# Optimization experiments

Hardware: AMD Instinct MI355X
Metric: run time of the kernel (lower is better)

The kernel has to match this reference:

```python
import jax, jax.numpy as jnp
import numpy as np

WINDOW_SIZE = 7
CHANNEL = 1
SIGMA = 1.5


def _create_window(window_size=WINDOW_SIZE, channel=CHANNEL):
    coords = jnp.arange(window_size, dtype=jnp.float32) - window_size // 2
    g = jnp.exp(-coords ** 2 / (2.0 * SIGMA ** 2))
    g = g / g.sum()
    w2d = g[:, None] * g[None, :]                      # [K, K]
    # depthwise kernel, OIHW with I=1 (groups=channel)
    return jnp.broadcast_to(w2d[None, None], (channel, 1, window_size, window_size))


def _dwconv(x, window):
    pad = WINDOW_SIZE // 2
    return jax.lax.conv_general_dilated(
        x, window,
        window_strides=(1, 1),
        padding=[(pad, pad), (pad, pad)],
        dimension_numbers=('NCHW', 'OIHW', 'NCHW'),
        feature_group_count=CHANNEL,
    )


def setup_inputs() -> dict:
    key = jax.random.key(0)
    k1, k2 = jax.random.split(key)
    shape = (128, CHANNEL, 256, 256)
    pred = jax.random.uniform(k1, shape, dtype=jnp.float32)
    target = jax.random.uniform(k2, shape, dtype=jnp.float32)
    window = _create_window()
    return {"pred": pred, "target": target, "window": window}


def reference(pred, target, window):
    C1 = 0.01 ** 2
    C2 = 0.03 ** 2
    mu1 = _dwconv(pred, window)
    mu2 = _dwconv(target, window)
    mu1_sq = mu1 * mu1
    mu2_sq = mu2 * mu2
    mu12 = mu1 * mu2
    sigma1_sq = _dwconv(pred * pred, window) - mu1_sq
    sigma2_sq = _dwconv(target * target, window) - mu2_sq
    sigma12 = _dwconv(pred * target, window) - mu12
    ssim_map = ((2.0 * mu12 + C1) * (2.0 * sigma12 + C2)) / (
        (mu1_sq + mu2_sq + C1) * (sigma1_sq + sigma2_sq + C2))
    return 1.0 - ssim_map.mean()
```

## Files before the change

kernel.cpp:

```cpp
#include <hip/hip_runtime.h>

#define IMG_H 256
#define IMG_W 256
#define ROWS 16
#define NIMG 128
#define NWAVES (NIMG * (IMG_H / ROWS) * 2)

__device__ __forceinline__ float ssim1(float mu1, float mu2, float spp, float stt, float spt) {
    const float C1 = 1e-4f, C2 = 9e-4f;
    float mu1s = mu1 * mu1, mu2s = mu2 * mu2, mu12 = mu1 * mu2;
    float s1 = spp - mu1s, s2 = stt - mu2s, s12 = spt - mu12;
    float num = (2.f * mu12 + C1) * (2.f * s12 + C2);
    float den = (mu1s + mu2s + C1) * (s1 + s2 + C2);
    return num * __builtin_amdgcn_rcpf(den);
}

template<int ATOMIC>
__global__ __launch_bounds__(256) void ssim_main(
    const float* __restrict__ pred,
    const float* __restrict__ targ,
    const float* __restrict__ window,
    float* __restrict__ wsum)
{
    __shared__ float2 sbuf[4][136];

    const int lane = threadIdx.x & 63;
    const int wid  = threadIdx.x >> 6;
    const int gw   = blockIdx.x * 4 + wid;
    const int n    = gw >> 5;
    const int r    = gw & 31;
    const int r0   = (r >> 1) * ROWS;
    const int X0   = (r & 1) << 7;

    float g[7];
    {
        float sum = 0.f;
#pragma unroll
        for (int j = 0; j < 7; ++j) { g[j] = window[21 + j]; sum += g[j]; }
        float inv = 1.f / sum;
#pragma unroll
        for (int j = 0; j < 7; ++j) g[j] *= inv;
    }

    const float* pimg = pred + (size_t)n * (IMG_H * IMG_W);
    const float* timg = targ + (size_t)n * (IMG_H * IMG_W);
    const int mo = X0 + 2 * lane;

    int hidx = 0, hcol = 0;
    if (lane < 3)      { hidx = lane + 1;   hcol = X0 - 3 + lane;   }
    else if (lane < 6) { hidx = lane + 129; hcol = X0 + 125 + lane; }
    const bool hv = (lane < 6) && ((unsigned)hcol < (unsigned)IMG_W);

    float Amu[7], Atu[7], App[7], Att[7], Apt[7];
    float Bmu[7], Btu[7], Bpp[7], Btt[7], Bpt[7];
    float acc = 0.f;

    float2 Pr, Tr, Hr;

#define GLOAD(J) { \
    const int j_ = (J); \
    Pr = make_float2(0.f, 0.f); Tr = Pr; Hr = Pr; \
    if ((unsigned)j_ < (unsigned)IMG_H) { \
        Pr = *(const float2*)(pimg + j_ * IMG_W + mo); \
        Tr = *(const float2*)(timg + j_ * IMG_W + mo); \
        if (hv) { \
            Hr.x = pimg[j_ * IMG_W + hcol]; \
            Hr.y = timg[j_ * IMG_W + hcol]; \
        } \
    } }

#define TAP(K, P, T) { \
    float wp = g[K] * (P), wt = g[K] * (T); \
    m_  = fmaf(g[K], (P), m_);  u_  = fmaf(g[K], (T), u_); \
    pp_ = fmaf(wp, (P), pp_);   tt_ = fmaf(wt, (T), tt_); \
    pt_ = fmaf(wp, (T), pt_); }

#define HC(SLOT, MU, TU, PP, TT, PT, p0,p1,p2,p3,p4,p5,p6, t0,t1,t2,t3,t4,t5,t6) { \
    float m_ = 0.f, u_ = 0.f, pp_ = 0.f, tt_ = 0.f, pt_ = 0.f; \
    TAP(0, p0, t0) TAP(1, p1, t1) TAP(2, p2, t2) TAP(3, p3, t3) \
    TAP(4, p4, t4) TAP(5, p5, t5) TAP(6, p6, t6) \
    MU[SLOT] = m_; TU[SLOT] = u_; PP[SLOT] = pp_; TT[SLOT] = tt_; PT[SLOT] = pt_; }

#define VD(A_, U) ( fmaf(g[6], A_[((U)+6)%7], fmaf(g[5], A_[((U)+5)%7], \
    fmaf(g[4], A_[((U)+4)%7], fmaf(g[3], A_[((U)+3)%7], fmaf(g[2], A_[((U)+2)%7], \
    fmaf(g[1], A_[((U)+1)%7], g[0] * A_[(U)%7])))))) )

#define OUTR(U) { \
    { float m1 = VD(Amu,U), m2 = VD(Atu,U), pp = VD(App,U), tt = VD(Att,U), pt = VD(Apt,U); \
      acc += ssim1(m1, m2, pp, tt, pt); } \
    { float m1 = VD(Bmu,U), m2 = VD(Btu,U), pp = VD(Bpp,U), tt = VD(Btt,U), pt = VD(Bpt,U); \
      acc += ssim1(m1, m2, pp, tt, pt); } }

#define STEPX(SLOT, JOFF, HASOUT, U, DOLOAD) { \
    { \
        float2* sw = sbuf[wid]; \
        *(float4*)(sw + 2 * lane + 4) = make_float4(Pr.x, Tr.x, Pr.y, Tr.y); \
        if (lane < 6) sw[hidx] = Hr; \
    } \
    const float2* sb = sbuf[wid]; \
    float4 q0 = *(const float4*)(sb + 2 * lane); \
    float4 q1 = *(const float4*)(sb + 2 * lane + 2); \
    float4 q2 = *(const float4*)(sb + 2 * lane + 4); \
    float4 q3 = *(const float4*)(sb + 2 * lane + 6); \
    float2 q4 = sb[2 * lane + 8]; \
    if (DOLOAD) { GLOAD(r0 + (JOFF) + 1); } \
    HC(SLOT, Amu, Atu, App, Att, Apt, \
       q0.z, q1.x, q1.z, q2.x, q2.z, q3.x, q3.z, \
       q0.w, q1.y, q1.w, q2.y, q2.w, q3.y, q3.w) \
    HC(SLOT, Bmu, Btu, Bpp, Btt, Bpt, \
       q1.x, q1.z, q2.x, q2.z, q3.x, q3.z, q4.x, \
       q1.y, q1.w, q2.y, q2.w, q3.y, q3.w, q4.y) \
    if (HASOUT) { OUTR(U) } }

    GLOAD(r0 - 3);

    STEPX(0, -3, 0, 0, 1)
    STEPX(1, -2, 0, 0, 1)
    STEPX(2, -1, 0, 0, 1)
    STEPX(3,  0, 0, 0, 1)
    STEPX(4,  1, 0, 0, 1)
    STEPX(5,  2, 0, 0, 1)

#pragma unroll 1
    for (int jb = 0; jb < 2; ++jb) {
        const int base = 3 + jb * 7;
        STEPX(6, base,     1, 0, 1)
        STEPX(0, base + 1, 1, 1, 1)
        STEPX(1, base + 2, 1, 2, 1)
        STEPX(2, base + 3, 1, 3, 1)
        STEPX(3, base + 4, 1, 4, 1)
        STEPX(4, base + 5, 1, 5, 1)
        STEPX(5, base + 6, 1, 6, 1)
    }
    STEPX(6, 17, 1, 0, 1)
    STEPX(0, 18, 1, 1, 0)

#undef GLOAD
#undef TAP
#undef HC
#undef VD
#undef OUTR
#undef STEPX

#pragma unroll
    for (int off = 32; off > 0; off >>= 1)
        acc += __shfl_xor(acc, off, 64);
    if (lane == 0) {
        if (ATOMIC) atomicAdd(&wsum[0], acc);
        else        wsum[gw] = acc;
    }
}

__global__ __launch_bounds__(256) void ssim_final_arr(
    const float* __restrict__ ws, float* __restrict__ out)
{
    __shared__ double sred[4];
    double sm = 0.0;
#pragma unroll
    for (int k = 0; k < NWAVES / 256; ++k)
        sm += (double)ws[threadIdx.x + k * 256];
#pragma unroll
    for (int off = 32; off > 0; off >>= 1)
        sm += __shfl_down(sm, off, 64);
    const int lane = threadIdx.x & 63, wid = threadIdx.x >> 6;
    if (lane == 0) sred[wid] = sm;
    __syncthreads();
    if (threadIdx.x == 0) {
        double tot = sred[0] + sred[1] + sred[2] + sred[3];
        out[0] = (float)(1.0 - tot * (1.0 / (128.0 * 256.0 * 256.0)));
    }
}

__global__ void ssim_final_sc(const float* __restrict__ ws, float* __restrict__ out)
{
    out[0] = 1.0f - ws[0] * (1.0f / (128.0f * 256.0f * 256.0f));
}

extern "C" void kernel_launch(void* const* d_in, const int* in_sizes, int n_in,
                              void* d_out, int out_size, void* d_ws, size_t ws_size,
                              hipStream_t stream)
{
    const float* pred   = (const float*)d_in[0];
    const float* targ   = (const float*)d_in[1];
    const float* window = (const float*)d_in[2];
    float* out = (float*)d_out;
    float* ws  = (float*)d_ws;

    if (ws_size >= NWAVES * sizeof(float)) {
        ssim_main<0><<<NWAVES / 4, 256, 0, stream>>>(pred, targ, window, ws);
        ssim_final_arr<<<1, 256, 0, stream>>>(ws, out);
    } else {
        hipMemsetAsync(ws, 0, sizeof(float), stream);
        ssim_main<1><<<NWAVES / 4, 256, 0, stream>>>(pred, targ, window, ws);
        ssim_final_sc<<<1, 1, 0, stream>>>(ws, out);
    }
    (void)in_sizes; (void)n_in; (void)out_size;
}
```

Baseline: 45.00 us.

## Give each wave one column per lane over a 64-wide strip

Each wave now covers a 64-column strip with one output column per lane instead of two, which doubles the number of waves. The second set of horizontal accumulators goes away and register pressure drops, so occupancy can rise. In exchange, halo loads and LDS traffic per output pixel go up, and each global load becomes a scalar float instead of a float2.

```diff
diff --git a/kernel.cpp b/kernel.cpp
--- a/kernel.cpp
+++ b/kernel.cpp
@@ -4,7 +4,7 @@
 #define IMG_W 256
 #define ROWS 16
 #define NIMG 128
-#define NWAVES (NIMG * (IMG_H / ROWS) * 2)
+#define NWAVES (NIMG * 64)
 
 __device__ __forceinline__ float ssim1(float mu1, float mu2, float spp, float stt, float spt) {
     const float C1 = 1e-4f, C2 = 9e-4f;
@@ -22,15 +22,15 @@
     const float* __restrict__ window,
     float* __restrict__ wsum)
 {
-    __shared__ float2 sbuf[4][136];
+    __shared__ float2 sbuf[4][72];
 
     const int lane = threadIdx.x & 63;
     const int wid  = threadIdx.x >> 6;
     const int gw   = blockIdx.x * 4 + wid;
-    const int n    = gw >> 5;
-    const int r    = gw & 31;
-    const int r0   = (r >> 1) * ROWS;
-    const int X0   = (r & 1) << 7;
+    const int n    = gw >> 6;
+    const int r    = gw & 63;
+    const int r0   = (r >> 2) * ROWS;
+    const int X0   = (r & 3) << 6;
 
     float g[7];
     {
@@ -44,25 +44,25 @@
 
     const float* pimg = pred + (size_t)n * (IMG_H * IMG_W);
     const float* timg = targ + (size_t)n * (IMG_H * IMG_W);
-    const int mo = X0 + 2 * lane;
+    const int mo = X0 + lane;
 
     int hidx = 0, hcol = 0;
-    if (lane < 3)      { hidx = lane + 1;   hcol = X0 - 3 + lane;   }
-    else if (lane < 6) { hidx = lane + 129; hcol = X0 + 125 + lane; }
+    if (lane < 3)      { hidx = lane + 1;  hcol = X0 - 3 + lane;  }
+    else if (lane < 6) { hidx = lane + 65; hcol = X0 + 61 + lane; }
     const bool hv = (lane < 6) && ((unsigned)hcol < (unsigned)IMG_W);
 
     float Amu[7], Atu[7], App[7], Att[7], Apt[7];
-    float Bmu[7], Btu[7], Bpp[7], Btt[7], Bpt[7];
     float acc = 0.f;
 
-    float2 Pr, Tr, Hr;
+    float Pr, Tr;
+    float2 Hr;
 
 #define GLOAD(J) { \
     const int j_ = (J); \
-    Pr = make_float2(0.f, 0.f); Tr = Pr; Hr = Pr; \
+    Pr = 0.f; Tr = 0.f; Hr = make_float2(0.f, 0.f); \
     if ((unsigned)j_ < (unsigned)IMG_H) { \
-        Pr = *(const float2*)(pimg + j_ * IMG_W + mo); \
-        Tr = *(const float2*)(timg + j_ * IMG_W + mo); \
+        Pr = pimg[j_ * IMG_W + mo]; \
+        Tr = timg[j_ * IMG_W + mo]; \
         if (hv) { \
             Hr.x = pimg[j_ * IMG_W + hcol]; \
             Hr.y = timg[j_ * IMG_W + hcol]; \
@@ -75,41 +75,33 @@
     pp_ = fmaf(wp, (P), pp_);   tt_ = fmaf(wt, (T), tt_); \
     pt_ = fmaf(wp, (T), pt_); }
 
-#define HC(SLOT, MU, TU, PP, TT, PT, p0,p1,p2,p3,p4,p5,p6, t0,t1,t2,t3,t4,t5,t6) { \
-    float m_ = 0.f, u_ = 0.f, pp_ = 0.f, tt_ = 0.f, pt_ = 0.f; \
-    TAP(0, p0, t0) TAP(1, p1, t1) TAP(2, p2, t2) TAP(3, p3, t3) \
-    TAP(4, p4, t4) TAP(5, p5, t5) TAP(6, p6, t6) \
-    MU[SLOT] = m_; TU[SLOT] = u_; PP[SLOT] = pp_; TT[SLOT] = tt_; PT[SLOT] = pt_; }
-
 #define VD(A_, U) ( fmaf(g[6], A_[((U)+6)%7], fmaf(g[5], A_[((U)+5)%7], \
     fmaf(g[4], A_[((U)+4)%7], fmaf(g[3], A_[((U)+3)%7], fmaf(g[2], A_[((U)+2)%7], \
     fmaf(g[1], A_[((U)+1)%7], g[0] * A_[(U)%7])))))) )
 
 #define OUTR(U) { \
-    { float m1 = VD(Amu,U), m2 = VD(Atu,U), pp = VD(App,U), tt = VD(Att,U), pt = VD(Apt,U); \
-      acc += ssim1(m1, m2, pp, tt, pt); } \
-    { float m1 = VD(Bmu,U), m2 = VD(Btu,U), pp = VD(Bpp,U), tt = VD(Btt,U), pt = VD(Bpt,U); \
-      acc += ssim1(m1, m2, pp, tt, pt); } }
+    float m1 = VD(Amu,U), m2 = VD(Atu,U), pp = VD(App,U), tt = VD(Att,U), pt = VD(Apt,U); \
+    acc += ssim1(m1, m2, pp, tt, pt); }
 
 #define STEPX(SLOT, JOFF, HASOUT, U, DOLOAD) { \
     { \
         float2* sw = sbuf[wid]; \
-        *(float4*)(sw + 2 * lane + 4) = make_float4(Pr.x, Tr.x, Pr.y, Tr.y); \
+        sw[lane + 4] = make_float2(Pr, Tr); \
         if (lane < 6) sw[hidx] = Hr; \
     } \
     const float2* sb = sbuf[wid]; \
-    float4 q0 = *(const float4*)(sb + 2 * lane); \
-    float4 q1 = *(const float4*)(sb + 2 * lane + 2); \
-    float4 q2 = *(const float4*)(sb + 2 * lane + 4); \
-    float4 q3 = *(const float4*)(sb + 2 * lane + 6); \
-    float2 q4 = sb[2 * lane + 8]; \
+    float2 q0 = sb[lane + 1], q1 = sb[lane + 2], q2 = sb[lane + 3]; \
+    float2 q3 = sb[lane + 4], q4 = sb[lane + 5], q5 = sb[lane + 6]; \
+    float2 q6 = sb[lane + 7]; \
     if (DOLOAD) { GLOAD(r0 + (JOFF) + 1); } \
-    HC(SLOT, Amu, Atu, App, Att, Apt, \
-       q0.z, q1.x, q1.z, q2.x, q2.z, q3.x, q3.z, \
-       q0.w, q1.y, q1.w, q2.y, q2.w, q3.y, q3.w) \
-    HC(SLOT, Bmu, Btu, Bpp, Btt, Bpt, \
-       q1.x, q1.z, q2.x, q2.z, q3.x, q3.z, q4.x, \
-       q1.y, q1.w, q2.y, q2.w, q3.y, q3.w, q4.y) \
+    { \
+        float m_ = 0.f, u_ = 0.f, pp_ = 0.f, tt_ = 0.f, pt_ = 0.f; \
+        TAP(0, q0.x, q0.y) TAP(1, q1.x, q1.y) TAP(2, q2.x, q2.y) \
+        TAP(3, q3.x, q3.y) TAP(4, q4.x, q4.y) TAP(5, q5.x, q5.y) \
+        TAP(6, q6.x, q6.y) \
+        Amu[SLOT] = m_; Atu[SLOT] = u_; App[SLOT] = pp_; \
+        Att[SLOT] = tt_; Apt[SLOT] = pt_; \
+    } \
     if (HASOUT) { OUTR(U) } }
 
     GLOAD(r0 - 3);
@@ -137,7 +129,6 @@
 
 #undef GLOAD
 #undef TAP
-#undef HC
 #undef VD
 #undef OUTR
 #undef STEPX
```

After: 44.64 us. No clear change (-0.8%).
